# Kernel tuning notes

Hardware: AMD Instinct MI355X
Metric: run time of the kernel (lower is better)

The kernel has to match this reference:

```python
import jax, jax.numpy as jnp
import numpy as np

K = 3
PAD = 1


def _deform_conv(x, offset, weight, bias):
    """torchvision-style deform_conv2d (v1, no mask), stride=1, pad=1, dil=1.
    x: [B,C,H,W], offset: [B,2*K*K,H,W] ordered (dy,dx) per kernel pos (row-major).
    """
    B, C, H, W = x.shape
    K2 = K * K
    off = offset.reshape(B, K2, 2, H, W)
    dy, dx = off[:, :, 0], off[:, :, 1]
    ky = jnp.repeat(jnp.arange(K), K).astype(x.dtype)  # [K2] kernel row offsets
    kx = jnp.tile(jnp.arange(K), K).astype(x.dtype)    # [K2] kernel col offsets
    hh = jnp.arange(H, dtype=x.dtype)
    ww = jnp.arange(W, dtype=x.dtype)
    # sampling positions: [B,K2,H,W]
    py = hh[None, None, :, None] + ky[None, :, None, None] - PAD + dy
    px = ww[None, None, None, :] + kx[None, :, None, None] - PAD + dx
    y0f = jnp.floor(py)
    x0f = jnp.floor(px)
    wy = py - y0f
    wx = px - x0f
    y0 = y0f.astype(jnp.int32)
    x0 = x0f.astype(jnp.int32)
    xf = x.reshape(B, C, H * W)

    def corner(iy, ix, w):
        # zero padding outside the image: contribution masked to 0
        valid = (iy >= 0) & (iy < H) & (ix >= 0) & (ix < W)
        iyc = jnp.clip(iy, 0, H - 1)
        ixc = jnp.clip(ix, 0, W - 1)
        lin = (iyc * W + ixc).reshape(B, -1)                      # [B,K2*H*W]
        g = jnp.take_along_axis(xf, lin[:, None, :], axis=2)     # [B,C,K2*H*W]
        g = g.reshape(B, C, K2, H, W)
        wv = (w * valid.astype(x.dtype))[:, None]                # [B,1,K2,H,W]
        return g * wv

    val = (corner(y0, x0, (1 - wy) * (1 - wx))
           + corner(y0, x0 + 1, (1 - wy) * wx)
           + corner(y0 + 1, x0, wy * (1 - wx))
           + corner(y0 + 1, x0 + 1, wy * wx))                    # [B,C,K2,H,W]
    O = weight.shape[0]
    out = jnp.einsum('ock,bckhw->bohw', weight.reshape(O, C, K2), val)
    return out + bias[None, :, None, None]


def setup_inputs() -> dict:
    key = jax.random.key(0)
    k1, k2, k3, k4, k5 = jax.random.split(key, 5)
    B, C, O, H, W = 4, 64, 64, 128, 128
    fan = C * K * K
    x = jax.random.normal(k1, (B, C, H, W), dtype=jnp.float32)
    w_off = jax.random.normal(k2, (2 * K * K, C, K, K), dtype=jnp.float32) / np.sqrt(fan)
    b_off = jax.random.normal(k3, (2 * K * K,), dtype=jnp.float32) * 0.01
    w_dcn = jax.random.normal(k4, (O, C, K, K), dtype=jnp.float32) / np.sqrt(fan)
    b_dcn = jax.random.normal(k5, (O,), dtype=jnp.float32) * 0.01
    return {"x": x, "w_off": w_off, "b_off": b_off, "w_dcn": w_dcn, "b_dcn": b_dcn}


def reference(x, w_off, b_off, w_dcn, b_dcn):
    offset = jax.lax.conv_general_dilated(
        x, w_off, window_strides=(1, 1), padding=((PAD, PAD), (PAD, PAD)),
        dimension_numbers=('NCHW', 'OIHW', 'NCHW')) + b_off[None, :, None, None]
    return _deform_conv(x, offset, w_dcn, b_dcn)
```

## Files before the change

### kernel.cpp

```cpp
#include <hip/hip_runtime.h>
#include <hip/hip_fp16.h>

#define HH 128
#define WW 128
#define CC 64
#define OO 64
#define HWSZ (HH*WW)

typedef _Float16 f16x8 __attribute__((ext_vector_type(8)));
typedef float    f32x4 __attribute__((ext_vector_type(4)));

__device__ __forceinline__ unsigned short f2h(float f) {
    return __half_as_ushort(__float2half_rn(f));
}

__global__ __launch_bounds__(256) void transpose_x(const float* __restrict__ x,
                                                   unsigned short* __restrict__ xh) {
    __shared__ float tile[64 * 65];
    int w0 = blockIdx.x * 64, h = blockIdx.y, b = blockIdx.z;
    int t = threadIdx.x;
    const float* xb = x + ((long)b * CC * HWSZ) + h * WW + w0;
#pragma unroll
    for (int i = 0; i < 16; ++i) {
        int idx = i * 256 + t; int c = idx >> 6, w = idx & 63;
        tile[c * 65 + w] = xb[c * HWSZ + w];
    }
    __syncthreads();
    unsigned short* xo = xh + ((long)((b * HH + h) * WW + w0)) * CC;
#pragma unroll
    for (int i = 0; i < 8; ++i) {
        int idx = i * 256 + t; int w = idx >> 5, c = (idx & 31) * 2;
        ushort2 u;
        u.x = f2h(tile[c * 65 + w]);
        u.y = f2h(tile[(c + 1) * 65 + w]);
        *(ushort2*)(xo + w * CC + c) = u;
    }
}

__global__ __launch_bounds__(256) void prep_w(const float* __restrict__ wd,
                                              const float* __restrict__ wo,
                                              unsigned short* __restrict__ wdtf,
                                              unsigned short* __restrict__ wotf) {
    int i = blockIdx.x * 256 + threadIdx.x;
    if (i < 36864) {
        int j = i & 7, l = (i >> 3) & 63, nt = (i >> 9) & 3, kcb = i >> 11;
        int k = kcb >> 1, cb = kcb & 1;
        int o = nt * 16 + (l & 15);
        int c = cb * 32 + ((l >> 4) & 3) * 8 + j;
        wdtf[i] = f2h(wd[(o * 64 + c) * 9 + k]);
    } else if (i < 36864 + 18432) {
        int jdx = i - 36864;
        int j = jdx & 7, l = (jdx >> 3) & 63, nt = (jdx >> 9) & 1, kcb = jdx >> 10;
        int k = kcb >> 1, cb = kcb & 1;
        int oc = nt * 16 + (l & 15);
        int c = cb * 32 + ((l >> 4) & 3) * 8 + j;
        wotf[jdx] = f2h(oc < 18 ? wo[(oc * 64 + c) * 9 + k] : 0.0f);
    }
}

__global__ __launch_bounds__(256) void offset_tile(const unsigned short* __restrict__ xh,
                                                   const unsigned short* __restrict__ wotf,
                                                   const float* __restrict__ b_off,
                                                   float* __restrict__ ofb) {
    __shared__ __attribute__((aligned(16))) unsigned short xr[3 * 68 * 72];
    int w0 = blockIdx.x * 64, h = blockIdx.y, b = blockIdx.z;
    int t = threadIdx.x;

#pragma unroll
    for (int i = 0; i < 7; ++i) {
        int idx = i * 256 + t;
        if (idx < 1584) {
            int r = idx / 528;
            int rem = idx - r * 528;
            int p = rem >> 3, cc = rem & 7;
            int y = h + r - 1, wx = w0 - 1 + p;
            uint4 v = make_uint4(0u, 0u, 0u, 0u);
            if (((unsigned)y < HH) && ((unsigned)wx < WW))
                v = *(const uint4*)(xh + ((long)((b * HH + y) * WW + wx)) * CC + cc * 8);
            *(uint4*)&xr[(r * 68 + p) * 72 + cc * 8] = v;
        }
    }
    __syncthreads();

    int l = t & 63, wv = t >> 6;
    int m = l & 15, q = l >> 4;
    int px0 = wv * 16;
    f32x4 acc0 = {0.f, 0.f, 0.f, 0.f}, acc1 = {0.f, 0.f, 0.f, 0.f};

#pragma unroll
    for (int k = 0; k < 9; ++k) {
        int ky = k / 3, kx = k - ky * 3;
        const unsigned short* ar = &xr[(ky * 68 + px0 + m + kx) * 72 + q * 8];
        f16x8 a0 = *(const f16x8*)(ar);
        f16x8 a1 = *(const f16x8*)(ar + 32);
        const unsigned short* bk = wotf + (k * 2) * 2 * 512 + l * 8;
        f16x8 b00 = *(const f16x8*)(bk);
        f16x8 b01 = *(const f16x8*)(bk + 512);
        f16x8 b10 = *(const f16x8*)(bk + 1024);
        f16x8 b11 = *(const f16x8*)(bk + 1536);
        acc0 = __builtin_amdgcn_mfma_f32_16x16x32_f16(a0, b00, acc0, 0, 0, 0);
        acc0 = __builtin_amdgcn_mfma_f32_16x16x32_f16(a1, b10, acc0, 0, 0, 0);
        acc1 = __builtin_amdgcn_mfma_f32_16x16x32_f16(a0, b01, acc1, 0, 0, 0);
        acc1 = __builtin_amdgcn_mfma_f32_16x16x32_f16(a1, b11, acc1, 0, 0, 0);
    }
    float* dst = ofb + ((long)((b * HH + h) * WW + w0 + px0)) * 18;
    float bo0 = b_off[m];
#pragma unroll
    for (int r = 0; r < 4; ++r)
        dst[(q * 4 + r) * 18 + m] = acc0[r] + bo0;
    if (m < 2) {
        float bo1 = b_off[16 + m];
#pragma unroll
        for (int r = 0; r < 4; ++r)
            dst[(q * 4 + r) * 18 + 16 + m] = acc1[r] + bo1;
    }
}

__global__ __launch_bounds__(256, 2) void deform_gemm(const unsigned short* __restrict__ xh,
                                                      const float* __restrict__ ofb,
                                                      const unsigned short* __restrict__ wdtf,
                                                      const float* __restrict__ b_dcn,
                                                      float* __restrict__ out) {
    __shared__ __attribute__((aligned(16))) unsigned short val_s[32 * 584];

    int w0 = blockIdx.x * 64, h = blockIdx.y, b = blockIdx.z;
    int t = threadIdx.x;
    int l = t & 63, wv = t >> 6;
    int m = l & 15, q = l >> 4;
    int spx = t >> 3, ch8 = t & 7;

    f16x8 Breg[18];
#pragma unroll
    for (int kc = 0; kc < 18; ++kc)
        Breg[kc] = *(const f16x8*)(wdtf + (kc * 4 + wv) * 512 + l * 8);

    const unsigned short* xb = xh + (long)b * HWSZ * CC;
    int o = wv * 16 + m;
    float bo = b_dcn[o];
    float* outo = out + ((long)(b * OO + o)) * HWSZ + h * WW;

#pragma unroll
    for (int g = 0; g < 2; ++g) {
        int wg0 = w0 + g * 32;
        const float* op = ofb + ((long)((b * HH + h) * WW + wg0 + spx)) * 18;
        float2 o9[9];
#pragma unroll
        for (int k = 0; k < 9; ++k) o9[k] = *(const float2*)(op + 2 * k);

#pragma unroll
        for (int k = 0; k < 9; ++k) {
            int ky = k / 3, kx = k - ky * 3;
            float py  = (float)(h + ky - 1) + o9[k].x;
            float pxf = (float)(wg0 + spx + kx - 1) + o9[k].y;
            float y0f = floorf(py), x0f = floorf(pxf);
            float wy = py - y0f, wx = pxf - x0f;
            int y0 = (int)y0f, x0 = (int)x0f, y1 = y0 + 1, x1 = x0 + 1;
            bool vy0 = (unsigned)y0 < HH, vy1 = (unsigned)y1 < HH;
            bool vx0 = (unsigned)x0 < WW, vx1 = (unsigned)x1 < WW;
            int y0c = min(max(y0, 0), HH - 1), y1c = min(max(y1, 0), HH - 1);
            int x0c = min(max(x0, 0), WW - 1), x1c = min(max(x1, 0), WW - 1);
            float cw0 = (vy0 && vx0) ? (1.f - wy) * (1.f - wx) : 0.f;
            float cw1 = (vy0 && vx1) ? (1.f - wy) * wx : 0.f;
            float cw2 = (vy1 && vx0) ? wy * (1.f - wx) : 0.f;
            float cw3 = (vy1 && vx1) ? wy * wx : 0.f;
            f16x8 s00 = *(const f16x8*)(xb + (y0c * WW + x0c) * CC + ch8 * 8);
            f16x8 s01 = *(const f16x8*)(xb + (y0c * WW + x1c) * CC + ch8 * 8);
            f16x8 s10 = *(const f16x8*)(xb + (y1c * WW + x0c) * CC + ch8 * 8);
            f16x8 s11 = *(const f16x8*)(xb + (y1c * WW + x1c) * CC + ch8 * 8);
            f16x8 a;
#pragma unroll
            for (int e = 0; e < 8; ++e) {
                float v = cw0 * (float)s00[e] + cw1 * (float)s01[e]
                        + cw2 * (float)s10[e] + cw3 * (float)s11[e];
                a[e] = (_Float16)v;
            }
            *(f16x8*)&val_s[spx * 584 + k * 64 + ch8 * 8] = a;
        }
        __syncthreads();

        f32x4 acc0 = {0.f, 0.f, 0.f, 0.f}, acc1 = {0.f, 0.f, 0.f, 0.f};
#pragma unroll
        for (int kc = 0; kc < 18; ++kc) {
            f16x8 a0 = *(const f16x8*)&val_s[m * 584 + kc * 32 + q * 8];
            f16x8 a1 = *(const f16x8*)&val_s[(16 + m) * 584 + kc * 32 + q * 8];
            acc0 = __builtin_amdgcn_mfma_f32_16x16x32_f16(a0, Breg[kc], acc0, 0, 0, 0);
            acc1 = __builtin_amdgcn_mfma_f32_16x16x32_f16(a1, Breg[kc], acc1, 0, 0, 0);
        }

        f32x4 r0 = acc0, r1 = acc1;
        r0[0] += bo; r0[1] += bo; r0[2] += bo; r0[3] += bo;
        r1[0] += bo; r1[1] += bo; r1[2] += bo; r1[3] += bo;
        *(f32x4*)(outo + wg0 + q * 4) = r0;
        *(f32x4*)(outo + wg0 + 16 + q * 4) = r1;
        __syncthreads();
    }
}

extern "C" void kernel_launch(void* const* d_in, const int* in_sizes, int n_in,
                              void* d_out, int out_size, void* d_ws, size_t ws_size,
                              hipStream_t stream) {
    const float* x     = (const float*)d_in[0];
    const float* w_off = (const float*)d_in[1];
    const float* b_off = (const float*)d_in[2];
    const float* w_dcn = (const float*)d_in[3];
    const float* b_dcn = (const float*)d_in[4];
    float* out = (float*)d_out;

    char* ws = (char*)d_ws;
    unsigned short* xh   = (unsigned short*)ws;
    float*          ofb  = (float*)(ws + 8388608);
    unsigned short* wdtf = (unsigned short*)(ws + 13107200);
    unsigned short* wotf = (unsigned short*)(ws + 13180928);

    hipLaunchKernelGGL(transpose_x, dim3(2, 128, 4), dim3(256), 0, stream, x, xh);
    hipLaunchKernelGGL(prep_w, dim3(216), dim3(256), 0, stream, w_dcn, w_off, wdtf, wotf);
    hipLaunchKernelGGL(offset_tile, dim3(2, 128, 4), dim3(256), 0, stream,
                       xh, wotf, b_off, ofb);
    hipLaunchKernelGGL(deform_gemm, dim3(2, 128, 4), dim3(256), 0, stream,
                       xh, ofb, wdtf, b_dcn, out);
}
```

Baseline: 114.7 us.

## Fuse offset conv into deform GEMM and merge prep kernels

Merges the weight-prep kernel into the x-transpose kernel as an extra grid slice, and fuses the offset convolution into the deform GEMM kernel. Offsets now stay in shared memory instead of round-tripping through a global buffer, which removes two launches and the offset store and reload. Bilinear interpolation now runs in packed fp16 arithmetic instead of fp32, which cuts VALU work but lowers accuracy. The fused kernel reuses one shared buffer for the input halo and the sampled values and needs more shared memory, so occupancy may drop.

After: 104.9 us. -8.6%, faster.

```diff
diff --git a/kernel.cpp b/kernel.cpp
--- a/kernel.cpp
+++ b/kernel.cpp
@@ -14,11 +14,33 @@
     return __half_as_ushort(__float2half_rn(f));
 }
 
-__global__ __launch_bounds__(256) void transpose_x(const float* __restrict__ x,
-                                                   unsigned short* __restrict__ xh) {
+__global__ __launch_bounds__(256) void prep_all(const float* __restrict__ x,
+                                                const float* __restrict__ wd,
+                                                const float* __restrict__ wo,
+                                                unsigned short* __restrict__ xh,
+                                                unsigned short* __restrict__ wdtf,
+                                                unsigned short* __restrict__ wotf) {
+    int t = threadIdx.x;
+    if (blockIdx.z == 4) {
+        int i = (blockIdx.y * 2 + blockIdx.x) * 256 + t;
+        if (i < 36864) {
+            int j = i & 7, l = (i >> 3) & 63, nt = (i >> 9) & 3, kcb = i >> 11;
+            int k = kcb >> 1, cb = kcb & 1;
+            int o = nt * 16 + (l & 15);
+            int c = cb * 32 + ((l >> 4) & 3) * 8 + j;
+            wdtf[i] = f2h(wd[(o * 64 + c) * 9 + k]);
+        } else if (i < 36864 + 18432) {
+            int jdx = i - 36864;
+            int j = jdx & 7, l = (jdx >> 3) & 63, nt = (jdx >> 9) & 1, kcb = jdx >> 10;
+            int k = kcb >> 1, cb = kcb & 1;
+            int oc = nt * 16 + (l & 15);
+            int c = cb * 32 + ((l >> 4) & 3) * 8 + j;
+            wotf[jdx] = f2h(oc < 18 ? wo[(oc * 64 + c) * 9 + k] : 0.0f);
+        }
+        return;
+    }
     __shared__ float tile[64 * 65];
     int w0 = blockIdx.x * 64, h = blockIdx.y, b = blockIdx.z;
-    int t = threadIdx.x;
     const float* xb = x + ((long)b * CC * HWSZ) + h * WW + w0;
 #pragma unroll
     for (int i = 0; i < 16; ++i) {
@@ -37,34 +59,21 @@
     }
 }
 
-__global__ __launch_bounds__(256) void prep_w(const float* __restrict__ wd,
-                                              const float* __restrict__ wo,
-                                              unsigned short* __restrict__ wdtf,
-                                              unsigned short* __restrict__ wotf) {
-    int i = blockIdx.x * 256 + threadIdx.x;
-    if (i < 36864) {
-        int j = i & 7, l = (i >> 3) & 63, nt = (i >> 9) & 3, kcb = i >> 11;
-        int k = kcb >> 1, cb = kcb & 1;
-        int o = nt * 16 + (l & 15);
-        int c = cb * 32 + ((l >> 4) & 3) * 8 + j;
-        wdtf[i] = f2h(wd[(o * 64 + c) * 9 + k]);
-    } else if (i < 36864 + 18432) {
-        int jdx = i - 36864;
-        int j = jdx & 7, l = (jdx >> 3) & 63, nt = (jdx >> 9) & 1, kcb = jdx >> 10;
-        int k = kcb >> 1, cb = kcb & 1;
-        int oc = nt * 16 + (l & 15);
-        int c = cb * 32 + ((l >> 4) & 3) * 8 + j;
-        wotf[jdx] = f2h(oc < 18 ? wo[(oc * 64 + c) * 9 + k] : 0.0f);
-    }
-}
-
-__global__ __launch_bounds__(256) void offset_tile(const unsigned short* __restrict__ xh,
-                                                   const unsigned short* __restrict__ wotf,
-                                                   const float* __restrict__ b_off,
-                                                   float* __restrict__ ofb) {
-    __shared__ __attribute__((aligned(16))) unsigned short xr[3 * 68 * 72];
+__global__ __launch_bounds__(256, 2) void fused_dcn(const unsigned short* __restrict__ xh,
+                                                    const unsigned short* __restrict__ wotf,
+                                                    const float* __restrict__ b_off,
+                                                    const unsigned short* __restrict__ wdtf,
+                                                    const float* __restrict__ b_dcn,
+                                                    float* __restrict__ out) {
+    __shared__ __attribute__((aligned(16))) unsigned short shm[32 * 584];
+    __shared__ float offs[64 * 20];
+    unsigned short* xr    = shm;
+    unsigned short* val_s = shm;
+
     int w0 = blockIdx.x * 64, h = blockIdx.y, b = blockIdx.z;
     int t = threadIdx.x;
+    int l = t & 63, wv = t >> 6;
+    int m = l & 15, q = l >> 4;
 
 #pragma unroll
     for (int i = 0; i < 7; ++i) {
@@ -81,52 +90,38 @@
         }
     }
     __syncthreads();
-
-    int l = t & 63, wv = t >> 6;
-    int m = l & 15, q = l >> 4;
-    int px0 = wv * 16;
-    f32x4 acc0 = {0.f, 0.f, 0.f, 0.f}, acc1 = {0.f, 0.f, 0.f, 0.f};
-
-#pragma unroll
-    for (int k = 0; k < 9; ++k) {
-        int ky = k / 3, kx = k - ky * 3;
-        const unsigned short* ar = &xr[(ky * 68 + px0 + m + kx) * 72 + q * 8];
-        f16x8 a0 = *(const f16x8*)(ar);
-        f16x8 a1 = *(const f16x8*)(ar + 32);
-        const unsigned short* bk = wotf + (k * 2) * 2 * 512 + l * 8;
-        f16x8 b00 = *(const f16x8*)(bk);
-        f16x8 b01 = *(const f16x8*)(bk + 512);
-        f16x8 b10 = *(const f16x8*)(bk + 1024);
-        f16x8 b11 = *(const f16x8*)(bk + 1536);
-        acc0 = __builtin_amdgcn_mfma_f32_16x16x32_f16(a0, b00, acc0, 0, 0, 0);
-        acc0 = __builtin_amdgcn_mfma_f32_16x16x32_f16(a1, b10, acc0, 0, 0, 0);
-        acc1 = __builtin_amdgcn_mfma_f32_16x16x32_f16(a0, b01, acc1, 0, 0, 0);
-        acc1 = __builtin_amdgcn_mfma_f32_16x16x32_f16(a1, b11, acc1, 0, 0, 0);
-    }
-    float* dst = ofb + ((long)((b * HH + h) * WW + w0 + px0)) * 18;
-    float bo0 = b_off[m];
-#pragma unroll
-    for (int r = 0; r < 4; ++r)
-        dst[(q * 4 + r) * 18 + m] = acc0[r] + bo0;
-    if (m < 2) {
-        float bo1 = b_off[16 + m];
+    {
+        int px0 = wv * 16;
+        f32x4 acc0 = {0.f, 0.f, 0.f, 0.f}, acc1 = {0.f, 0.f, 0.f, 0.f};
+#pragma unroll
+        for (int k = 0; k < 9; ++k) {
+            int ky = k / 3, kx = k - ky * 3;
+            const unsigned short* ar = &xr[(ky * 68 + px0 + m + kx) * 72 + q * 8];
+            f16x8 a0 = *(const f16x8*)(ar);
+            f16x8 a1 = *(const f16x8*)(ar + 32);
+            const unsigned short* bk = wotf + (k * 2) * 2 * 512 + l * 8;
+            f16x8 b00 = *(const f16x8*)(bk);
+            f16x8 b01 = *(const f16x8*)(bk + 512);
+            f16x8 b10 = *(const f16x8*)(bk + 1024);
+            f16x8 b11 = *(const f16x8*)(bk + 1536);
+            acc0 = __builtin_amdgcn_mfma_f32_16x16x32_f16(a0, b00, acc0, 0, 0, 0);
+            acc0 = __builtin_amdgcn_mfma_f32_16x16x32_f16(a1, b10, acc0, 0, 0, 0);
+            acc1 = __builtin_amdgcn_mfma_f32_16x16x32_f16(a0, b01, acc1, 0, 0, 0);
+            acc1 = __builtin_amdgcn_mfma_f32_16x16x32_f16(a1, b11, acc1, 0, 0, 0);
+        }
+        float bo0 = b_off[m];
 #pragma unroll
         for (int r = 0; r < 4; ++r)
-            dst[(q * 4 + r) * 18 + 16 + m] = acc1[r] + bo1;
-    }
-}
-
-__global__ __launch_bounds__(256, 2) void deform_gemm(const unsigned short* __restrict__ xh,
-                                                      const float* __restrict__ ofb,
-                                                      const unsigned short* __restrict__ wdtf,
-                                                      const float* __restrict__ b_dcn,
-                                                      float* __restrict__ out) {
-    __shared__ __attribute__((aligned(16))) unsigned short val_s[32 * 584];
-
-    int w0 = blockIdx.x * 64, h = blockIdx.y, b = blockIdx.z;
-    int t = threadIdx.x;
-    int l = t & 63, wv = t >> 6;
-    int m = l & 15, q = l >> 4;
+            offs[(px0 + q * 4 + r) * 20 + m] = acc0[r] + bo0;
+        if (m < 2) {
+            float bo1 = b_off[16 + m];
+#pragma unroll
+            for (int r = 0; r < 4; ++r)
+                offs[(px0 + q * 4 + r) * 20 + 16 + m] = acc1[r] + bo1;
+        }
+    }
+    __syncthreads();
+
     int spx = t >> 3, ch8 = t & 7;
 
     f16x8 Breg[18];
@@ -142,16 +137,14 @@
 #pragma unroll
     for (int g = 0; g < 2; ++g) {
         int wg0 = w0 + g * 32;
-        const float* op = ofb + ((long)((b * HH + h) * WW + wg0 + spx)) * 18;
-        float2 o9[9];
-#pragma unroll
-        for (int k = 0; k < 9; ++k) o9[k] = *(const float2*)(op + 2 * k);
+        const float* oprow = &offs[(g * 32 + spx) * 20];
 
 #pragma unroll
         for (int k = 0; k < 9; ++k) {
             int ky = k / 3, kx = k - ky * 3;
-            float py  = (float)(h + ky - 1) + o9[k].x;
-            float pxf = (float)(wg0 + spx + kx - 1) + o9[k].y;
+            float2 ov = *(const float2*)(oprow + 2 * k);
+            float py  = (float)(h + ky - 1) + ov.x;
+            float pxf = (float)(wg0 + spx + kx - 1) + ov.y;
             float y0f = floorf(py), x0f = floorf(pxf);
             float wy = py - y0f, wx = pxf - x0f;
             int y0 = (int)y0f, x0 = (int)x0f, y1 = y0 + 1, x1 = x0 + 1;
@@ -159,21 +152,15 @@
             bool vx0 = (unsigned)x0 < WW, vx1 = (unsigned)x1 < WW;
             int y0c = min(max(y0, 0), HH - 1), y1c = min(max(y1, 0), HH - 1);
             int x0c = min(max(x0, 0), WW - 1), x1c = min(max(x1, 0), WW - 1);
-            float cw0 = (vy0 && vx0) ? (1.f - wy) * (1.f - wx) : 0.f;
-            float cw1 = (vy0 && vx1) ? (1.f - wy) * wx : 0.f;
-            float cw2 = (vy1 && vx0) ? wy * (1.f - wx) : 0.f;
-            float cw3 = (vy1 && vx1) ? wy * wx : 0.f;
+            _Float16 h0 = (_Float16)((vy0 && vx0) ? (1.f - wy) * (1.f - wx) : 0.f);
+            _Float16 h1 = (_Float16)((vy0 && vx1) ? (1.f - wy) * wx : 0.f);
+            _Float16 h2 = (_Float16)((vy1 && vx0) ? wy * (1.f - wx) : 0.f);
+            _Float16 h3 = (_Float16)((vy1 && vx1) ? wy * wx : 0.f);
             f16x8 s00 = *(const f16x8*)(xb + (y0c * WW + x0c) * CC + ch8 * 8);
             f16x8 s01 = *(const f16x8*)(xb + (y0c * WW + x1c) * CC + ch8 * 8);
             f16x8 s10 = *(const f16x8*)(xb + (y1c * WW + x0c) * CC + ch8 * 8);
             f16x8 s11 = *(const f16x8*)(xb + (y1c * WW + x1c) * CC + ch8 * 8);
-            f16x8 a;
-#pragma unroll
-            for (int e = 0; e < 8; ++e) {
-                float v = cw0 * (float)s00[e] + cw1 * (float)s01[e]
-                        + cw2 * (float)s10[e] + cw3 * (float)s11[e];
-                a[e] = (_Float16)v;
-            }
+            f16x8 a = s00 * h0 + s01 * h1 + s10 * h2 + s11 * h3;
             *(f16x8*)&val_s[spx * 584 + k * 64 + ch8 * 8] = a;
         }
         __syncthreads();
@@ -208,14 +195,11 @@
 
     char* ws = (char*)d_ws;
     unsigned short* xh   = (unsigned short*)ws;
-    float*          ofb  = (float*)(ws + 8388608);
-    unsigned short* wdtf = (unsigned short*)(ws + 13107200);
-    unsigned short* wotf = (unsigned short*)(ws + 13180928);
-
-    hipLaunchKernelGGL(transpose_x, dim3(2, 128, 4), dim3(256), 0, stream, x, xh);
-    hipLaunchKernelGGL(prep_w, dim3(216), dim3(256), 0, stream, w_dcn, w_off, wdtf, wotf);
-    hipLaunchKernelGGL(offset_tile, dim3(2, 128, 4), dim3(256), 0, stream,
-                       xh, wotf, b_off, ofb);
-    hipLaunchKernelGGL(deform_gemm, dim3(2, 128, 4), dim3(256), 0, stream,
-                       xh, ofb, wdtf, b_dcn, out);
-}
+    unsigned short* wdtf = (unsigned short*)(ws + 8388608);
+    unsigned short* wotf = (unsigned short*)(ws + 8462336);
+
+    hipLaunchKernelGGL(prep_all, dim3(2, 128, 5), dim3(256), 0, stream,
+                       x, w_dcn, w_off, xh, wdtf, wotf);
+    hipLaunchKernelGGL(fused_dcn, dim3(2, 128, 4), dim3(256), 0, stream,
+                       xh, wotf, b_off, wdtf, b_dcn, out);
+}
```
